# Kernel tuning notes

Measured on AMD Instinct MI355X. Metric: run time of the kernel, lower is better.

The kernel has to match this reference:

```python
import jax, jax.numpy as jnp
import numpy as np

N_USERS = 50000
N_ENTITIES = 250000
N_RELATIONS = 24
EMBED_DIM = 128
RELATION_DIM = 128
KG_BATCH = 16384
KG_L2_LAMBDA = 1e-5


def _l2_loss_mean(x):
    # mean over batch of (||x||^2 / 2)
    return jnp.mean(jnp.sum(x * x, axis=1) / 2.0)


def setup_inputs() -> dict:
    key = jax.random.key(0)
    k1, k2, k3, k4, k5, k6, k7 = jax.random.split(key, 7)
    n_total = N_ENTITIES + N_USERS
    # xavier-uniform-like init scale
    s_e = float(np.sqrt(6.0 / (n_total + EMBED_DIM)))
    s_r = float(np.sqrt(6.0 / (N_RELATIONS + RELATION_DIM)))
    s_m = float(np.sqrt(6.0 / (EMBED_DIM + RELATION_DIM)))
    entity_user_embed = jax.random.uniform(k1, (n_total, EMBED_DIM), jnp.float32, -s_e, s_e)
    relation_embed = jax.random.uniform(k2, (N_RELATIONS, RELATION_DIM), jnp.float32, -s_r, s_r)
    trans_M = jax.random.uniform(k3, (N_RELATIONS, EMBED_DIM, RELATION_DIM), jnp.float32, -s_m, s_m)
    h = jax.random.randint(k4, (KG_BATCH,), 0, n_total, dtype=jnp.int64 if jax.config.jax_enable_x64 else jnp.int32)
    r = jax.random.randint(k5, (KG_BATCH,), 0, N_RELATIONS, dtype=h.dtype)
    pos_t = jax.random.randint(k6, (KG_BATCH,), 0, n_total, dtype=h.dtype)
    neg_t = jax.random.randint(k7, (KG_BATCH,), 0, n_total, dtype=h.dtype)
    return {
        "entity_user_embed": entity_user_embed,
        "relation_embed": relation_embed,
        "trans_M": trans_M,
        "h": h,
        "r": r,
        "pos_t": pos_t,
        "neg_t": neg_t,
    }


def reference(entity_user_embed, relation_embed, trans_M, h, r, pos_t, neg_t):
    # KGAT.calc_kg_loss (mode='train_kg')
    r_embed = relation_embed[r]            # [B, R]
    W_r = trans_M[r]                       # [B, E, R] per-edge TransR matrix (gather)
    h_embed = entity_user_embed[h]         # [B, E]
    pos_t_embed = entity_user_embed[pos_t] # [B, E]
    neg_t_embed = entity_user_embed[neg_t] # [B, E]

    # bmm([B,1,E], [B,E,R]) -> [B,R]
    r_mul_h = jnp.einsum('be,ber->br', h_embed, W_r)
    r_mul_pos_t = jnp.einsum('be,ber->br', pos_t_embed, W_r)
    r_mul_neg_t = jnp.einsum('be,ber->br', neg_t_embed, W_r)

    pos_score = jnp.sum(jnp.square(r_mul_h + r_embed - r_mul_pos_t), axis=1)
    neg_score = jnp.sum(jnp.square(r_mul_h + r_embed - r_mul_neg_t), axis=1)

    kg_loss = jnp.mean(-jax.nn.log_sigmoid(neg_score - pos_score))
    l2_loss = (_l2_loss_mean(r_mul_h) + _l2_loss_mean(r_embed)
               + _l2_loss_mean(r_mul_pos_t) + _l2_loss_mean(r_mul_neg_t))
    return kg_loss + KG_L2_LAMBDA * l2_loss
```

## Files before the change

### kernel.cpp

```cpp
#include <hip/hip_runtime.h>
#include <math.h>

#define KG_B    16384
#define KG_D    128
#define KG_NR   24
#define KG_TM   32
#define KG_BPAD (KG_B + KG_NR * KG_TM)
#define KG_NGRP (KG_BPAD / KG_TM)

#define WS_BSUM KG_BPAD
#define WS_PREW_BYTES 131072

typedef __attribute__((ext_vector_type(8))) short bf16x8;
typedef __attribute__((ext_vector_type(4))) float f32x4;

__device__ __forceinline__ unsigned bf16r(float f) {
    return (__float_as_uint(f) + 0x8000u) >> 16;
}
__device__ __forceinline__ unsigned pack2(float lo, float hi) {
    return bf16r(lo) | (bf16r(hi) << 16);
}

__global__ __launch_bounds__(1024) void kg_sort_prep(const int* __restrict__ r,
                                                     const float* __restrict__ M,
                                                     int* __restrict__ perm,
                                                     unsigned short* __restrict__ preW) {
    __shared__ int cntw[16][25];
    __shared__ int basew[16][25];
    __shared__ int pbase_s[24];
    __shared__ int cnt_tot[24];
    __shared__ int total_s;
    __shared__ __align__(16) unsigned short sWp[KG_D * KG_D];

    const int t = threadIdx.x;

    if (blockIdx.x != 0) {
        const int k  = blockIdx.x - 1;
        const int e  = t >> 3;
        const int c0 = (t & 7) * 16;
        const float* src = M + ((size_t)k << 14) + (size_t)e * KG_D + c0;
        float4 rw[4];
#pragma unroll
        for (int f = 0; f < 4; ++f) rw[f] = ((const float4*)src)[f];
#pragma unroll
        for (int dc = 0; dc < 16; ++dc) {
            const int col = c0 + dc;
            const float v = ((const float*)&rw[0])[dc];
            sWp[col * KG_D + e] = (unsigned short)bf16r(v);
        }
        __syncthreads();
        uint4* dst = (uint4*)(preW + ((size_t)k << 14));
        const uint4* s4 = (const uint4*)sWp;
        dst[2 * t]     = s4[2 * t];
        dst[2 * t + 1] = s4[2 * t + 1];
        return;
    }

    const int w = t >> 6;
    int* cz = &cntw[0][0];
    for (int i = t; i < 16 * 25; i += 1024) cz[i] = 0;
    __syncthreads();

    int kt[16];
#pragma unroll
    for (int j = 0; j < 16; ++j) kt[j] = r[j * 1024 + t];
#pragma unroll
    for (int j = 0; j < 16; ++j) atomicAdd(&cntw[w][kt[j]], 1);
    __syncthreads();

    if (t < 24) {
        int s = 0;
        for (int w2 = 0; w2 < 16; ++w2) { basew[w2][t] = s; s += cntw[w2][t]; }
        cnt_tot[t] = s;
    }
    __syncthreads();
    if (t == 0) {
        int run = 0;
        for (int k = 0; k < 24; ++k) {
            pbase_s[k] = run;
            run += (cnt_tot[k] + (KG_TM - 1)) & ~(KG_TM - 1);
        }
        total_s = run;
    }
    __syncthreads();
    if (t < 24)
        for (int w2 = 0; w2 < 16; ++w2) basew[w2][t] += pbase_s[t];
    for (int i = t; i < 16 * 25; i += 1024) cz[i] = 0;
    __syncthreads();

#pragma unroll
    for (int j = 0; j < 16; ++j) {
        const int k = kt[j];
        const int pos = basew[w][k] + atomicAdd(&cntw[w][k], 1);
        perm[pos] = j * 1024 + t;
    }
    __syncthreads();

    if (t < 24) {
        const int e0 = pbase_s[t] + cnt_tot[t];
        const int e1 = pbase_s[t] + ((cnt_tot[t] + (KG_TM - 1)) & ~(KG_TM - 1));
        for (int p = e0; p < e1; ++p) perm[p] = -1;
    }
    for (int i = total_s + t; i < KG_BPAD; i += 1024) perm[i] = -1;
}

__global__ __launch_bounds__(256, 3) void kg_main(
    const float* __restrict__ ent, const float* __restrict__ rel,
    const unsigned short* __restrict__ preW,
    const int* __restrict__ h,     const int* __restrict__ r,
    const int* __restrict__ pt,    const int* __restrict__ nt,
    const int* __restrict__ perm,  float* __restrict__ bsum)
{
    __shared__ __align__(16) unsigned short sX[3 * KG_TM * KG_D];
    __shared__ float sScr[2][KG_TM][4];

    const int tid   = threadIdx.x;
    const int slot0 = blockIdx.x * KG_TM;
    const int p0    = perm[slot0];
    if (p0 < 0) {
        if (tid == 0) bsum[blockIdx.x] = 0.f;
        return;
    }
    const int rb = __builtin_amdgcn_readfirstlane(r[p0]);

    const int l   = tid & 63;
    const int wv  = tid >> 6;
    const int rt  = wv & 1;
    const int chs = wv >> 1;
    const int li  = l & 15;
    const int kq  = l >> 4;

    const unsigned short* __restrict__ preWk = preW + ((size_t)rb << 14);
    bf16x8 bpre[4][4];
#pragma unroll
    for (int kk = 0; kk < 4; ++kk)
#pragma unroll
        for (int n = 0; n < 4; ++n)
            bpre[kk][n] = *(const bf16x8*)&preWk[(chs * 64 + n * 16 + li) * KG_D
                                                 + kk * 32 + kq * 8];
    const float* relrow = rel + (size_t)rb * KG_D + chs * 64;
    float relv[4];
#pragma unroll
    for (int n = 0; n < 4; ++n) relv[n] = relrow[n * 16 + li];

    {
        const int g  = tid >> 3;
        const int e0 = (tid & 7) * 16;
        const int pg = perm[slot0 + g];
        const int bb = pg < 0 ? p0 : pg;
        const int idx3[3] = { h[bb], pt[bb], nt[bb] };
        const int sw = (g & 7) << 3;
#pragma unroll
        for (int t3 = 0; t3 < 3; ++t3) {
            const float* src = ent + (size_t)idx3[t3] * KG_D + e0;
            const float4 f0 = ((const float4*)src)[0];
            const float4 f1 = ((const float4*)src)[1];
            const float4 f2 = ((const float4*)src)[2];
            const float4 f3 = ((const float4*)src)[3];
            uint4 u0, u1;
            u0.x = pack2(f0.x, f0.y); u0.y = pack2(f0.z, f0.w);
            u0.z = pack2(f1.x, f1.y); u0.w = pack2(f1.z, f1.w);
            u1.x = pack2(f2.x, f2.y); u1.y = pack2(f2.z, f2.w);
            u1.z = pack2(f3.x, f3.y); u1.w = pack2(f3.z, f3.w);
            unsigned short* base = sX + t3 * (KG_TM * KG_D) + g * KG_D;
            *(uint4*)(base + ((e0    ) ^ sw)) = u0;
            *(uint4*)(base + ((e0 + 8) ^ sw)) = u1;
        }
    }
    __syncthreads();

    const int ar  = rt * 16 + li;
    const int asw = (ar & 7) << 3;

    f32x4 accf[3][4];
#pragma unroll
    for (int t3 = 0; t3 < 3; ++t3)
#pragma unroll
        for (int n = 0; n < 4; ++n) accf[t3][n] = (f32x4)0.f;

#pragma unroll
    for (int kk = 0; kk < 4; ++kk) {
        const int e0 = kk * 32 + kq * 8;
        bf16x8 af[3];
#pragma unroll
        for (int t3 = 0; t3 < 3; ++t3)
            af[t3] = *(const bf16x8*)&sX[t3 * (KG_TM * KG_D) + ar * KG_D + (e0 ^ asw)];
#pragma unroll
        for (int n = 0; n < 4; ++n) {
            accf[0][n] = __builtin_amdgcn_mfma_f32_16x16x32_bf16(af[0], bpre[kk][n], accf[0][n], 0, 0, 0);
            accf[1][n] = __builtin_amdgcn_mfma_f32_16x16x32_bf16(af[1], bpre[kk][n], accf[1][n], 0, 0, 0);
            accf[2][n] = __builtin_amdgcn_mfma_f32_16x16x32_bf16(af[2], bpre[kk][n], accf[2][n], 0, 0, 0);
        }
    }

    float ps[4] = {0,0,0,0}, ns[4] = {0,0,0,0}, sq[4] = {0,0,0,0};
#pragma unroll
    for (int n = 0; n < 4; ++n) {
        const float rv = relv[n];
#pragma unroll
        for (int j = 0; j < 4; ++j) {
            const float va = accf[0][n][j];
            const float vp = accf[1][n][j];
            const float vn = accf[2][n][j];
            const float s  = va + rv;
            const float dp = s - vp;
            const float dn = s - vn;
            ps[j] += dp * dp;
            ns[j] += dn * dn;
            sq[j] += va * va + vp * vp + vn * vn + rv * rv;
        }
    }
#pragma unroll
    for (int j = 0; j < 4; ++j)
#pragma unroll
        for (int m = 1; m < 16; m <<= 1) {
            ps[j] += __shfl_xor(ps[j], m);
            ns[j] += __shfl_xor(ns[j], m);
            sq[j] += __shfl_xor(sq[j], m);
        }

    if (li == 0) {
#pragma unroll
        for (int j = 0; j < 4; ++j) {
            const int row = rt * 16 + kq * 4 + j;
            sScr[chs][row][0] = ps[j];
            sScr[chs][row][1] = ns[j];
            sScr[chs][row][2] = sq[j];
        }
    }
    __syncthreads();

    if (tid < 64) {
        float term = 0.f;
        if (tid < KG_TM) {
            const int row = tid;
            const float P = sScr[0][row][0] + sScr[1][row][0];
            const float N = sScr[0][row][1] + sScr[1][row][1];
            const float S = sScr[0][row][2] + sScr[1][row][2];
            const int pg = perm[slot0 + row];
            if (pg >= 0) {
                const float x = P - N;
                term = fmaxf(x, 0.f) + log1pf(expf(-fabsf(x)))
                     + 5e-6f * S;
            }
        }
#pragma unroll
        for (int off = 16; off > 0; off >>= 1) term += __shfl_down(term, off);
        if (tid == 0) bsum[blockIdx.x] = term;
    }
}

__global__ __launch_bounds__(256) void kg_final(const float* __restrict__ bsum,
                                                float* __restrict__ out) {
    __shared__ float s[256];
    const int t = threadIdx.x;
    float acc = 0.f;
    for (int i = t; i < KG_NGRP; i += 256) acc += bsum[i];
    s[t] = acc;
    __syncthreads();
    for (int off = 128; off > 0; off >>= 1) {
        if (t < off) s[t] += s[t + off];
        __syncthreads();
    }
    if (t == 0) out[0] = s[0] * (1.0f / (float)KG_B);
}

extern "C" void kernel_launch(void* const* d_in, const int* in_sizes, int n_in,
                              void* d_out, int out_size, void* d_ws, size_t ws_size,
                              hipStream_t stream) {
    const float* ent = (const float*)d_in[0];
    const float* rel = (const float*)d_in[1];
    const float* M   = (const float*)d_in[2];
    const int*   h   = (const int*)d_in[3];
    const int*   r   = (const int*)d_in[4];
    const int*   pt  = (const int*)d_in[5];
    const int*   nt  = (const int*)d_in[6];

    int*            perm = (int*)d_ws;
    float*          bsum = (float*)d_ws + WS_BSUM;
    unsigned short* preW = (unsigned short*)((char*)d_ws + WS_PREW_BYTES);
    float*          out  = (float*)d_out;

    kg_sort_prep<<<1 + KG_NR, 1024, 0, stream>>>(r, M, perm, preW);
    kg_main     <<<KG_NGRP, 256, 0, stream>>>(ent, rel, preW, h, r, pt, nt, perm, bsum);
    kg_final    <<<1, 256, 0, stream>>>(bsum, out);
}
```

Measured before the change: 28.53 us.

## Split relation counting sort across 16 blocks with histogram and ballot-based scatter

Replaces the single-block counting sort over relation ids with a two-kernel scheme. The first kernel has 16 blocks that each build a partial histogram, and it still does the bf16 weight pretranspose. The second kernel has 16 blocks that scatter indices using wave ballots and popcount ranks, so no shared atomics are needed. The goal is to remove the serial single-block sort that sits on the critical path before the main kernel. The cost is an extra kernel launch and a global round trip for the partial counts.

Measured after the change: 27.87 us. 2.3% less time.

```diff
diff --git a/kernel.cpp b/kernel.cpp
--- a/kernel.cpp
+++ b/kernel.cpp
@@ -7,8 +7,10 @@
 #define KG_TM   32
 #define KG_BPAD (KG_B + KG_NR * KG_TM)
 #define KG_NGRP (KG_BPAD / KG_TM)
-
-#define WS_BSUM KG_BPAD
+#define KG_HB   16
+
+#define WS_BSUM     KG_BPAD
+#define WS_CNTPART  (KG_BPAD + KG_NGRP)
 #define WS_PREW_BYTES 131072
 
 typedef __attribute__((ext_vector_type(8))) short bf16x8;
@@ -21,21 +23,16 @@
     return bf16r(lo) | (bf16r(hi) << 16);
 }
 
-__global__ __launch_bounds__(1024) void kg_sort_prep(const int* __restrict__ r,
+__global__ __launch_bounds__(1024) void kg_hist_prep(const int* __restrict__ r,
                                                      const float* __restrict__ M,
                                                      int* __restrict__ perm,
+                                                     int* __restrict__ cntpart,
                                                      unsigned short* __restrict__ preW) {
-    __shared__ int cntw[16][25];
-    __shared__ int basew[16][25];
-    __shared__ int pbase_s[24];
-    __shared__ int cnt_tot[24];
-    __shared__ int total_s;
-    __shared__ __align__(16) unsigned short sWp[KG_D * KG_D];
-
     const int t = threadIdx.x;
 
-    if (blockIdx.x != 0) {
-        const int k  = blockIdx.x - 1;
+    if (blockIdx.x >= KG_HB) {
+        __shared__ __align__(16) unsigned short sWp[KG_D * KG_D];
+        const int k  = blockIdx.x - KG_HB;
         const int e  = t >> 3;
         const int c0 = (t & 7) * 16;
         const float* src = M + ((size_t)k << 14) + (size_t)e * KG_D + c0;
@@ -56,52 +53,64 @@
         return;
     }
 
-    const int w = t >> 6;
-    int* cz = &cntw[0][0];
-    for (int i = t; i < 16 * 25; i += 1024) cz[i] = 0;
-    __syncthreads();
-
-    int kt[16];
-#pragma unroll
-    for (int j = 0; j < 16; ++j) kt[j] = r[j * 1024 + t];
-#pragma unroll
-    for (int j = 0; j < 16; ++j) atomicAdd(&cntw[w][kt[j]], 1);
+    __shared__ int hc[24];
+    const int j = blockIdx.x;
+    if (t < 24) hc[t] = 0;
+    for (int i = j * 1024 + t; i < KG_BPAD; i += KG_HB * 1024) perm[i] = -1;
+    __syncthreads();
+    atomicAdd(&hc[r[j * 1024 + t]], 1);
+    __syncthreads();
+    if (t < 24) cntpart[j * 32 + t] = hc[t];
+}
+
+__global__ __launch_bounds__(1024) void kg_scatter(const int* __restrict__ r,
+                                                   const int* __restrict__ cntpart,
+                                                   int* __restrict__ perm) {
+    __shared__ int wcnt[16][25];
+    __shared__ int wbase[16][25];
+    __shared__ int tot[24], myb[24], pb0[24];
+
+    const int j    = blockIdx.x;
+    const int t    = threadIdx.x;
+    const int w    = t >> 6;
+    const int lane = t & 63;
+
+    const int k = r[j * 1024 + t];
+
+    unsigned long long mym = 0;
+#pragma unroll
+    for (int b = 0; b < 24; ++b) {
+        const unsigned long long m = __ballot(k == b);
+        if (k == b) mym = m;
+        if (lane == 0) wcnt[w][b] = (int)__popcll(m);
+    }
+    const int rank_w = (int)__popcll(mym & ((1ull << lane) - 1ull));
     __syncthreads();
 
     if (t < 24) {
         int s = 0;
-        for (int w2 = 0; w2 < 16; ++w2) { basew[w2][t] = s; s += cntw[w2][t]; }
-        cnt_tot[t] = s;
+        for (int w2 = 0; w2 < 16; ++w2) { wbase[w2][t] = s; s += wcnt[w2][t]; }
+        int s2 = 0, mb = 0;
+        for (int j2 = 0; j2 < KG_HB; ++j2) {
+            const int c = cntpart[j2 * 32 + t];
+            s2 += c;
+            if (j2 < j) mb += c;
+        }
+        tot[t] = s2;
+        myb[t] = mb;
     }
     __syncthreads();
     if (t == 0) {
         int run = 0;
-        for (int k = 0; k < 24; ++k) {
-            pbase_s[k] = run;
-            run += (cnt_tot[k] + (KG_TM - 1)) & ~(KG_TM - 1);
-        }
-        total_s = run;
-    }
-    __syncthreads();
-    if (t < 24)
-        for (int w2 = 0; w2 < 16; ++w2) basew[w2][t] += pbase_s[t];
-    for (int i = t; i < 16 * 25; i += 1024) cz[i] = 0;
-    __syncthreads();
-
-#pragma unroll
-    for (int j = 0; j < 16; ++j) {
-        const int k = kt[j];
-        const int pos = basew[w][k] + atomicAdd(&cntw[w][k], 1);
-        perm[pos] = j * 1024 + t;
-    }
-    __syncthreads();
-
-    if (t < 24) {
-        const int e0 = pbase_s[t] + cnt_tot[t];
-        const int e1 = pbase_s[t] + ((cnt_tot[t] + (KG_TM - 1)) & ~(KG_TM - 1));
-        for (int p = e0; p < e1; ++p) perm[p] = -1;
-    }
-    for (int i = total_s + t; i < KG_BPAD; i += 1024) perm[i] = -1;
+        for (int k2 = 0; k2 < 24; ++k2) {
+            pb0[k2] = run;
+            run += (tot[k2] + (KG_TM - 1)) & ~(KG_TM - 1);
+        }
+    }
+    __syncthreads();
+
+    const int pos = pb0[k] + myb[k] + wbase[w][k] + rank_w;
+    perm[pos] = j * 1024 + t;
 }
 
 __global__ __launch_bounds__(256, 3) void kg_main(
@@ -276,12 +285,14 @@
     const int*   pt  = (const int*)d_in[5];
     const int*   nt  = (const int*)d_in[6];
 
-    int*            perm = (int*)d_ws;
-    float*          bsum = (float*)d_ws + WS_BSUM;
-    unsigned short* preW = (unsigned short*)((char*)d_ws + WS_PREW_BYTES);
-    float*          out  = (float*)d_out;
-
-    kg_sort_prep<<<1 + KG_NR, 1024, 0, stream>>>(r, M, perm, preW);
+    int*            perm    = (int*)d_ws;
+    float*          bsum    = (float*)d_ws + WS_BSUM;
+    int*            cntpart = (int*)d_ws + WS_CNTPART;
+    unsigned short* preW    = (unsigned short*)((char*)d_ws + WS_PREW_BYTES);
+    float*          out     = (float*)d_out;
+
+    kg_hist_prep<<<KG_HB + KG_NR, 1024, 0, stream>>>(r, M, perm, cntpart, preW);
+    kg_scatter  <<<KG_HB, 1024, 0, stream>>>(r, cntpart, perm);
     kg_main     <<<KG_NGRP, 256, 0, stream>>>(ent, rel, preW, h, r, pt, nt, perm, bsum);
     kg_final    <<<1, 256, 0, stream>>>(bsum, out);
 }
```
